# Kernel optimization log

Measured on AMD Instinct MI355X. Metric: run time of the kernel, lower is better.

Reference implementation:

```python
import jax, jax.numpy as jnp
import numpy as np

B, S, D = 4, 2048, 1024
H, DK, DV = 16, 64, 64
LN_EPS = 1e-5


def setup_inputs() -> dict:
    key = jax.random.key(0)
    ks = jax.random.split(key, 16)
    s = 0.02
    inp = {
        "Q": jax.random.normal(ks[0], (B, S, D), jnp.float32),
        "K": jax.random.normal(ks[1], (B, S, D), jnp.float32),
        "V": jax.random.normal(ks[2], (B, S, D), jnp.float32),
        "mask": jnp.tril(jnp.ones((S, S), jnp.int32)),  # causal 2D mask
        "W_Q": jax.random.normal(ks[3], (D, H * DK), jnp.float32) * s,
        "b_Q": jnp.zeros((H * DK,), jnp.float32),
        "W_K": jax.random.normal(ks[4], (D, H * DK), jnp.float32) * s,
        "b_K": jnp.zeros((H * DK,), jnp.float32),
        "W_V": jax.random.normal(ks[5], (D, H * DV), jnp.float32) * s,
        "b_V": jnp.zeros((H * DV,), jnp.float32),
        "W_O": jax.random.normal(ks[6], (H * DV, D), jnp.float32) * s,
        "b_O": jnp.zeros((D,), jnp.float32),
        "ln_gamma": jnp.ones((D,), jnp.float32),
        "ln_beta": jnp.zeros((D,), jnp.float32),
    }
    return inp


def reference(Q, K, V, mask, W_Q, b_Q, W_K, b_K, W_V, b_V, W_O, b_O, ln_gamma, ln_beta):
    residual = Q
    # projections -> [B, H, S, d]
    q = (Q @ W_Q + b_Q).reshape(B, S, H, DK).transpose(0, 2, 1, 3)
    k = (K @ W_K + b_K).reshape(B, S, H, DK).transpose(0, 2, 1, 3)
    v = (V @ W_V + b_V).reshape(B, S, H, DV).transpose(0, 2, 1, 3)
    # scaled dot-product attention with explicit [B,H,S,S] scores
    scores = jnp.einsum("bhqd,bhkd->bhqk", q, k) / jnp.sqrt(jnp.float32(DK))
    m = mask[None, None, :, :]  # 2D mask -> [1,1,S,S] as in torch code
    scores = jnp.where(m == 0, jnp.float32(-1e9), scores)
    attn = jax.nn.softmax(scores, axis=-1)
    out = jnp.einsum("bhqk,bhkd->bhqd", attn, v)
    out = out.transpose(0, 2, 1, 3).reshape(B, S, H * DV)
    out = out @ W_O + b_O
    # layer norm over residual + out
    x = residual + out
    mu = jnp.mean(x, axis=-1, keepdims=True)
    var = jnp.mean(jnp.square(x - mu), axis=-1, keepdims=True)
    y = (x - mu) / jnp.sqrt(var + LN_EPS) * ln_gamma + ln_beta
    return y, attn
```

## Files before the change

### kernel.cpp

```cpp
#include <hip/hip_runtime.h>
#include <hip/hip_bf16.h>
#include <math.h>

#define NB 4
#define NS 2048
#define ND 1024
#define NH 16

typedef __attribute__((ext_vector_type(8))) __bf16 bf16x8;
typedef __attribute__((ext_vector_type(4))) float f32x4;
typedef __attribute__((ext_vector_type(8))) unsigned short ushort8_t;

#define VMCNT0() asm volatile("s_waitcnt vmcnt(0)" ::: "memory")
#define VMCNT2() asm volatile("s_waitcnt vmcnt(2)" ::: "memory")
#define VMCNT4() asm volatile("s_waitcnt vmcnt(4)" ::: "memory")
#define LGKM0()  asm volatile("s_waitcnt lgkmcnt(0)" ::: "memory")
#define BAR()    __builtin_amdgcn_s_barrier()

__device__ __forceinline__ unsigned short f2bf(float f){
  union { float f; unsigned int u; } v; v.f = f;
  unsigned int r = (v.u + 0x7FFFu + ((v.u >> 16) & 1u)) >> 16;
  return (unsigned short)r;
}
__device__ __forceinline__ float bf2f(unsigned short u){
  union { unsigned int i; float f; } v; v.i = ((unsigned int)u) << 16;
  return v.f;
}
__device__ __forceinline__ f32x4 mfma16(bf16x8 a, bf16x8 b, f32x4 c){
  return __builtin_amdgcn_mfma_f32_16x16x32_bf16(a, b, c, 0, 0, 0);
}
__device__ __forceinline__ bf16x8 lds_frag(const unsigned short* p){
  ushort8_t u = *reinterpret_cast<const ushort8_t*>(p);
  return __builtin_bit_cast(bf16x8, u);
}
__device__ __forceinline__ void gl16(const unsigned short* g, unsigned short* l){
  __builtin_amdgcn_global_load_lds(
      (const __attribute__((address_space(1))) void*)g,
      (__attribute__((address_space(3))) void*)l, 16, 0, 0);
}

__global__ __launch_bounds__(256)
void k_convert3(const float* __restrict__ a, const float* __restrict__ b,
                const float* __restrict__ c, unsigned short* __restrict__ oa,
                unsigned short* __restrict__ ob, unsigned short* __restrict__ oc,
                int n4){
  int i = blockIdx.x * 256 + threadIdx.x;
  if (i >= n4) return;
  const float* in = (blockIdx.y == 0) ? a : (blockIdx.y == 1) ? b : c;
  unsigned short* out = (blockIdx.y == 0) ? oa : (blockIdx.y == 1) ? ob : oc;
  float4 v = reinterpret_cast<const float4*>(in)[i];
  ushort4 o;
  o.x = f2bf(v.x); o.y = f2bf(v.y); o.z = f2bf(v.z); o.w = f2bf(v.w);
  reinterpret_cast<ushort4*>(out)[i] = o;
}

__global__ __launch_bounds__(256)
void k_transpose4(const float* __restrict__ w0, const float* __restrict__ w1,
                  const float* __restrict__ w2, const float* __restrict__ w3,
                  unsigned short* __restrict__ out){
  __shared__ float t[32][33];
  const float* in = (blockIdx.z == 0) ? w0 : (blockIdx.z == 1) ? w1 :
                    (blockIdx.z == 2) ? w2 : w3;
  unsigned short* o = out + (size_t)blockIdx.z * 1048576;
  const int k0 = blockIdx.x * 32, n0 = blockIdx.y * 32;
  const int tx = threadIdx.x & 31, ty = threadIdx.x >> 5;
  for (int r = ty; r < 32; r += 8)
    t[r][tx] = in[(size_t)(k0 + r) * 1024 + n0 + tx];
  __syncthreads();
  for (int r = ty; r < 32; r += 8)
    o[(size_t)(n0 + r) * 1024 + k0 + tx] = f2bf(t[tx][r]);
}

__global__ __launch_bounds__(256)
void k_gemm_qkv(const unsigned short* __restrict__ A0,
                const unsigned short* __restrict__ A1,
                const unsigned short* __restrict__ A2,
                const unsigned short* __restrict__ WT,
                const float* __restrict__ b0, const float* __restrict__ b1,
                const float* __restrict__ b2,
                unsigned short* __restrict__ o0,
                unsigned short* __restrict__ o1,
                unsigned short* __restrict__ o2)
{
  constexpr int K = 1024;
  __shared__ unsigned short a_s[128 * 64];
  __shared__ unsigned short b_s[128 * 64];
  const int bm = blockIdx.x;
  const int gid = blockIdx.y >> 3, bn = blockIdx.y & 7;
  const unsigned short* A = (gid == 0) ? A0 : (gid == 1) ? A1 : A2;
  const unsigned short* BT = WT + (size_t)gid * 1048576;
  const float* bias = (gid == 0) ? b0 : (gid == 1) ? b1 : b2;
  unsigned short* outp = (gid == 0) ? o0 : (gid == 1) ? o1 : o2;

  const int tid = threadIdx.x, lane = tid & 63, w = tid >> 6;
  const int wr = w >> 1, wc = w & 1;
  const int l15 = lane & 15, l4 = lane >> 4;
  const int xsw = (l15 & 7) << 3;
  const int lr = lane >> 3;
  const int scol = ((lane & 7) << 3) ^ (lr << 3);

  const f32x4 z4 = {0.f, 0.f, 0.f, 0.f};
  f32x4 acc[4][4];
  #pragma unroll
  for (int i = 0; i < 4; ++i)
    #pragma unroll
    for (int j = 0; j < 4; ++j) acc[i][j] = z4;

  const size_t abase = (size_t)(bm * 128) * K;
  const size_t bbase = (size_t)(bn * 128) * K;

  for (int kt = 0; kt < 16; ++kt){
    __syncthreads();
    #pragma unroll
    for (int i = 0; i < 4; ++i){
      const int row = w * 32 + i * 8 + lr;
      gl16(&A[abase + (size_t)row * K + kt * 64 + scol], &a_s[(w * 32 + i * 8) * 64]);
      gl16(&BT[bbase + (size_t)row * K + kt * 64 + scol], &b_s[(w * 32 + i * 8) * 64]);
    }
    __syncthreads();
    #pragma unroll
    for (int ks = 0; ks < 2; ++ks){
      const int cb = (ks * 32 + l4 * 8) ^ xsw;
      bf16x8 af[4], bfr[4];
      #pragma unroll
      for (int mf = 0; mf < 4; ++mf)
        af[mf] = lds_frag(&a_s[(wr * 64 + mf * 16 + l15) * 64 + cb]);
      #pragma unroll
      for (int nf = 0; nf < 4; ++nf)
        bfr[nf] = lds_frag(&b_s[(wc * 64 + nf * 16 + l15) * 64 + cb]);
      #pragma unroll
      for (int mf = 0; mf < 4; ++mf)
        #pragma unroll
        for (int nf = 0; nf < 4; ++nf)
          acc[mf][nf] = mfma16(af[mf], bfr[nf], acc[mf][nf]);
    }
  }

  #pragma unroll
  for (int mf = 0; mf < 4; ++mf){
    #pragma unroll
    for (int nf = 0; nf < 4; ++nf){
      const int n = bn * 128 + wc * 64 + nf * 16 + l15;
      const float bv = bias[n];
      #pragma unroll
      for (int r = 0; r < 4; ++r){
        const int m = bm * 128 + wr * 64 + mf * 16 + l4 * 4 + r;
        const float v = acc[mf][nf][r] + bv;
        const int b = m >> 11, s = m & 2047, h = n >> 6, d = n & 63;
        if (gid <= 1)
          outp[((((size_t)b * NH + h) * NS + s) << 6) + d] = f2bf(v);
        else
          outp[(((size_t)b * NH + h) * 64 + d) * NS + s] = f2bf(v);
      }
    }
  }
}

__global__ __launch_bounds__(256)
void k_gemm_o(const unsigned short* __restrict__ A,
              const unsigned short* __restrict__ BT,
              const float* __restrict__ bias,
              const float* __restrict__ resid,
              unsigned short* __restrict__ outp)
{
  constexpr int K = 1024;
  __shared__ unsigned short a_s[128 * 64];
  __shared__ unsigned short b_s[128 * 64];
  const int bm = blockIdx.x, bn = blockIdx.y;
  const int tid = threadIdx.x, lane = tid & 63, w = tid >> 6;
  const int wr = w >> 1, wc = w & 1;
  const int l15 = lane & 15, l4 = lane >> 4;
  const int xsw = (l15 & 7) << 3;
  const int lr = lane >> 3;
  const int scol = ((lane & 7) << 3) ^ (lr << 3);

  const f32x4 z4 = {0.f, 0.f, 0.f, 0.f};
  f32x4 acc[4][4];
  #pragma unroll
  for (int i = 0; i < 4; ++i)
    #pragma unroll
    for (int j = 0; j < 4; ++j) acc[i][j] = z4;

  const size_t abase = (size_t)(bm * 128) * K;
  const size_t bbase = (size_t)(bn * 128) * K;

  for (int kt = 0; kt < 16; ++kt){
    __syncthreads();
    #pragma unroll
    for (int i = 0; i < 4; ++i){
      const int row = w * 32 + i * 8 + lr;
      gl16(&A[abase + (size_t)row * K + kt * 64 + scol], &a_s[(w * 32 + i * 8) * 64]);
      gl16(&BT[bbase + (size_t)row * K + kt * 64 + scol], &b_s[(w * 32 + i * 8) * 64]);
    }
    __syncthreads();
    #pragma unroll
    for (int ks = 0; ks < 2; ++ks){
      const int cb = (ks * 32 + l4 * 8) ^ xsw;
      bf16x8 af[4], bfr[4];
      #pragma unroll
      for (int mf = 0; mf < 4; ++mf)
        af[mf] = lds_frag(&a_s[(wr * 64 + mf * 16 + l15) * 64 + cb]);
      #pragma unroll
      for (int nf = 0; nf < 4; ++nf)
        bfr[nf] = lds_frag(&b_s[(wc * 64 + nf * 16 + l15) * 64 + cb]);
      #pragma unroll
      for (int mf = 0; mf < 4; ++mf)
        #pragma unroll
        for (int nf = 0; nf < 4; ++nf)
          acc[mf][nf] = mfma16(af[mf], bfr[nf], acc[mf][nf]);
    }
  }

  #pragma unroll
  for (int mf = 0; mf < 4; ++mf){
    #pragma unroll
    for (int nf = 0; nf < 4; ++nf){
      const int n = bn * 128 + wc * 64 + nf * 16 + l15;
      const float bv = bias[n];
      #pragma unroll
      for (int r = 0; r < 4; ++r){
        const int m = bm * 128 + wr * 64 + mf * 16 + l4 * 4 + r;
        const size_t idx = (size_t)m * ND + n;
        outp[idx] = f2bf(acc[mf][nf][r] + bv + resid[idx]);
      }
    }
  }
}

__global__ __launch_bounds__(256, 4)
void k_attn(const unsigned short* __restrict__ qh,
            const unsigned short* __restrict__ kh,
            const unsigned short* __restrict__ vt,
            unsigned short* __restrict__ ctx,
            float* __restrict__ attn)
{
  __shared__ unsigned short k_s0[64 * 64];
  __shared__ unsigned short k_s1[64 * 64];
  __shared__ unsigned short kv2[64 * 64];
  __shared__ unsigned short p_s[64][72];

  const int id = blockIdx.x + 32 * blockIdx.y;
  const int swz = (id & 7) * 256 + (id >> 3);
  const int bh = swz >> 5;
  const int qb = 31 - (swz & 31);
  const int q0 = qb * 64;
  const int tid = threadIdx.x, lane = tid & 63, w = tid >> 6;
  const int l15 = lane & 15, l4 = lane >> 4;
  const int xsw = (l15 & 7) << 3;
  const int lr = lane >> 3;
  const int scol = ((lane & 7) << 3) ^ (lr << 3);
  const f32x4 z4 = {0.f, 0.f, 0.f, 0.f};
  const size_t kvb = (size_t)bh * NS * 64;

  bf16x8 qf[2];
  {
    const unsigned short* qp = &qh[kvb + (size_t)(q0 + w * 16 + l15) * 64];
    qf[0] = lds_frag(qp + l4 * 8);
    qf[1] = lds_frag(qp + 32 + l4 * 8);
  }

  const float SC = 0.125f * 1.44269504088896341f;
  const int ncomp = qb + 1;
  const int growb = q0 + w * 16 + l4 * 4;

  float lp[4] = {0.f, 0.f, 0.f, 0.f};

  #pragma unroll
  for (int i = 0; i < 2; ++i)
    gl16(&kh[kvb + (size_t)(w * 16 + i * 8 + lr) * 64 + scol],
         &k_s0[(w * 16 + i * 8) * 64]);
  if (ncomp > 1){
    #pragma unroll
    for (int i = 0; i < 2; ++i)
      gl16(&kh[kvb + (size_t)(64 + w * 16 + i * 8 + lr) * 64 + scol],
           &k_s1[(w * 16 + i * 8) * 64]);
    VMCNT2();
  } else {
    VMCNT0();
  }
  BAR();

  int cbi = 0;
  for (int kt = 0; kt < ncomp; ++kt){
    const bool haveNext = (kt + 1 < ncomp);
    const bool havePre  = (kt + 2 < ncomp);
    if (havePre){
      int nbi = cbi + 2; if (nbi >= 3) nbi -= 3;
      unsigned short* nb = (nbi == 0) ? k_s0 : ((nbi == 1) ? k_s1 : kv2);
      #pragma unroll
      for (int i = 0; i < 2; ++i)
        gl16(&kh[kvb + (size_t)((kt + 2) * 64 + w * 16 + i * 8 + lr) * 64 + scol],
             &nb[(w * 16 + i * 8) * 64]);
    }
    const unsigned short* cb_ = (cbi == 0) ? k_s0 : ((cbi == 1) ? k_s1 : kv2);
    f32x4 sc4[4];
    #pragma unroll
    for (int cf = 0; cf < 4; ++cf) sc4[cf] = z4;
    __builtin_amdgcn_s_setprio(1);
    #pragma unroll
    for (int ks = 0; ks < 2; ++ks){
      const int cb = (ks * 32 + l4 * 8) ^ xsw;
      #pragma unroll
      for (int cf = 0; cf < 4; ++cf){
        const bf16x8 bk = lds_frag(&cb_[(cf * 16 + l15) * 64 + cb]);
        sc4[cf] = mfma16(qf[ks], bk, sc4[cf]);
      }
    }
    __builtin_amdgcn_s_setprio(0);
    if (kt == ncomp - 1){
      #pragma unroll
      for (int cf = 0; cf < 4; ++cf){
        const int gcol = kt * 64 + cf * 16 + l15;
        #pragma unroll
        for (int r = 0; r < 4; ++r)
          lp[r] += (gcol <= growb + r) ? exp2f(sc4[cf][r] * SC) : 0.f;
      }
    } else {
      #pragma unroll
      for (int cf = 0; cf < 4; ++cf)
        #pragma unroll
        for (int r = 0; r < 4; ++r)
          lp[r] += exp2f(sc4[cf][r] * SC);
    }
    if (havePre){ VMCNT2(); } else if (haveNext){ VMCNT0(); }
    LGKM0();
    BAR();
    cbi = (cbi == 2) ? 0 : cbi + 1;
  }

  float rl[4];
  #pragma unroll
  for (int r = 0; r < 4; ++r){
    float t = lp[r];
    t += __shfl_xor(t, 1);
    t += __shfl_xor(t, 2);
    t += __shfl_xor(t, 4);
    t += __shfl_xor(t, 8);
    rl[r] = 1.f / t;
  }

  f32x4 oacc[4];
  #pragma unroll
  for (int nf = 0; nf < 4; ++nf) oacc[nf] = z4;
  float* arow = attn + (size_t)bh * NS * NS;

  #pragma unroll
  for (int i = 0; i < 2; ++i)
    gl16(&kh[kvb + (size_t)(w * 16 + i * 8 + lr) * 64 + scol],
         &k_s0[(w * 16 + i * 8) * 64]);
  VMCNT0();
  BAR();
  int cur = 0;

  for (int kt = 0; kt < ncomp; ++kt){
    const bool haveK = (kt + 1 < ncomp);
    unsigned short* kcur = cur ? k_s1 : k_s0;
    unsigned short* knxt = cur ? k_s0 : k_s1;
    #pragma unroll
    for (int i = 0; i < 2; ++i){
      const int row = w * 16 + i * 8 + lr;
      gl16(&vt[kvb + (size_t)row * NS + kt * 64 + scol], &kv2[(w * 16 + i * 8) * 64]);
    }
    if (haveK){
      #pragma unroll
      for (int i = 0; i < 2; ++i)
        gl16(&kh[kvb + (size_t)((kt + 1) * 64 + w * 16 + i * 8 + lr) * 64 + scol],
             &knxt[(w * 16 + i * 8) * 64]);
    }
    f32x4 sc4[4];
    #pragma unroll
    for (int cf = 0; cf < 4; ++cf) sc4[cf] = z4;
    __builtin_amdgcn_s_setprio(1);
    #pragma unroll
    for (int ks = 0; ks < 2; ++ks){
      const int cb = (ks * 32 + l4 * 8) ^ xsw;
      #pragma unroll
      for (int cf = 0; cf < 4; ++cf){
        const bf16x8 bk = lds_frag(&kcur[(cf * 16 + l15) * 64 + cb]);
        sc4[cf] = mfma16(qf[ks], bk, sc4[cf]);
      }
    }
    __builtin_amdgcn_s_setprio(0);
    if (kt == ncomp - 1){
      #pragma unroll
      for (int cf = 0; cf < 4; ++cf){
        const int gcol = kt * 64 + cf * 16 + l15;
        #pragma unroll
        for (int r = 0; r < 4; ++r){
          const float a = (gcol <= growb + r) ? exp2f(sc4[cf][r] * SC) * rl[r] : 0.f;
          p_s[w * 16 + l4 * 4 + r][cf * 16 + l15] = f2bf(a);
        }
      }
    } else {
      #pragma unroll
      for (int cf = 0; cf < 4; ++cf)
        #pragma unroll
        for (int r = 0; r < 4; ++r)
          p_s[w * 16 + l4 * 4 + r][cf * 16 + l15] = f2bf(exp2f(sc4[cf][r] * SC) * rl[r]);
    }
    if (haveK){ VMCNT2(); } else { VMCNT0(); }
    LGKM0();
    BAR();
    #pragma unroll
    for (int it = 0; it < 4; ++it){
      const int row = it * 16 + (tid >> 4);
      const int c0 = (tid & 15) * 4;
      const ushort4 u = *reinterpret_cast<const ushort4*>(&p_s[row][c0]);
      float4 f4;
      f4.x = bf2f(u.x); f4.y = bf2f(u.y); f4.z = bf2f(u.z); f4.w = bf2f(u.w);
      *reinterpret_cast<float4*>(&arow[(size_t)(q0 + row) * NS + kt * 64 + c0]) = f4;
    }
    __builtin_amdgcn_s_setprio(1);
    #pragma unroll
    for (int ks2 = 0; ks2 < 2; ++ks2){
      const bf16x8 ap = lds_frag(&p_s[w * 16 + l15][ks2 * 32 + l4 * 8]);
      const int cb = (ks2 * 32 + l4 * 8) ^ xsw;
      #pragma unroll
      for (int nf = 0; nf < 4; ++nf){
        const bf16x8 bv = lds_frag(&kv2[(nf * 16 + l15) * 64 + cb]);
        oacc[nf] = mfma16(ap, bv, oacc[nf]);
      }
    }
    __builtin_amdgcn_s_setprio(0);
    if (haveK){
      VMCNT4();
      BAR();
    }
    cur ^= 1;
  }

  const int b = bh >> 4, h = bh & 15;
  #pragma unroll
  for (int nf = 0; nf < 4; ++nf){
    #pragma unroll
    for (int r = 0; r < 4; ++r){
      const int s = growb + r;
      ctx[((size_t)b * NS + s) * ND + h * 64 + nf * 16 + l15] = f2bf(oacc[nf][r]);
    }
  }

  const int zc0 = ncomp * 64;
  if (zc0 < NS){
    const float4 zz = make_float4(0.f, 0.f, 0.f, 0.f);
    for (int r = 0; r < 64; ++r){
      float* rp = arow + (size_t)(q0 + r) * NS;
      for (int c = zc0 + tid * 4; c < NS; c += 1024)
        *reinterpret_cast<float4*>(rp + c) = zz;
    }
  }
}

__global__ __launch_bounds__(256)
void k_ln(const unsigned short* __restrict__ x, const float* __restrict__ gamma,
          const float* __restrict__ beta, float* __restrict__ y){
  const int row = blockIdx.x;
  const ushort4 u = reinterpret_cast<const ushort4*>(x + (size_t)row * ND)[threadIdx.x];
  float v0 = bf2f(u.x), v1 = bf2f(u.y), v2 = bf2f(u.z), v3 = bf2f(u.w);
  float s = v0 + v1 + v2 + v3;
  float ss = v0 * v0 + v1 * v1 + v2 * v2 + v3 * v3;
  #pragma unroll
  for (int off = 32; off; off >>= 1){
    s += __shfl_xor(s, off);
    ss += __shfl_xor(ss, off);
  }
  __shared__ float rs[4], rss[4];
  const int w = threadIdx.x >> 6;
  if ((threadIdx.x & 63) == 0){ rs[w] = s; rss[w] = ss; }
  __syncthreads();
  s = rs[0] + rs[1] + rs[2] + rs[3];
  ss = rss[0] + rss[1] + rss[2] + rss[3];
  const float mu = s * (1.f / ND);
  const float var = ss * (1.f / ND) - mu * mu;
  const float rstd = rsqrtf(var + 1e-5f);
  const float4 g = reinterpret_cast<const float4*>(gamma)[threadIdx.x];
  const float4 be = reinterpret_cast<const float4*>(beta)[threadIdx.x];
  float4 o;
  o.x = (v0 - mu) * rstd * g.x + be.x;
  o.y = (v1 - mu) * rstd * g.y + be.y;
  o.z = (v2 - mu) * rstd * g.z + be.z;
  o.w = (v3 - mu) * rstd * g.w + be.w;
  reinterpret_cast<float4*>(y + (size_t)row * ND)[threadIdx.x] = o;
}

extern "C" void kernel_launch(void* const* d_in, const int* in_sizes, int n_in,
                              void* d_out, int out_size, void* d_ws, size_t ws_size,
                              hipStream_t stream){
  const float* Q   = (const float*)d_in[0];
  const float* Kin = (const float*)d_in[1];
  const float* V   = (const float*)d_in[2];
  const float* W_Q = (const float*)d_in[4];
  const float* b_Q = (const float*)d_in[5];
  const float* W_K = (const float*)d_in[6];
  const float* b_K = (const float*)d_in[7];
  const float* W_V = (const float*)d_in[8];
  const float* b_V = (const float*)d_in[9];
  const float* W_O = (const float*)d_in[10];
  const float* b_O = (const float*)d_in[11];
  const float* g   = (const float*)d_in[12];
  const float* be  = (const float*)d_in[13];

  char* ws = (char*)d_ws;
  const size_t SZ = (size_t)8192 * 1024 * 2;
  unsigned short* Qb = (unsigned short*)(ws);
  unsigned short* Kb = (unsigned short*)(ws + SZ);
  unsigned short* Vb = (unsigned short*)(ws + 2 * SZ);
  unsigned short* WT = (unsigned short*)(ws + 3 * SZ);
  unsigned short* qh = (unsigned short*)(ws + 3 * SZ + 4 * 2097152);
  unsigned short* kh = qh + (size_t)8388608;
  unsigned short* vt = kh + (size_t)8388608;
  unsigned short* ctx = Qb;
  unsigned short* x = Kb;
  float* y = (float*)d_out;
  float* attn = y + (size_t)NB * NS * ND;

  const int n4 = (NB * NS * ND) / 4;
  k_convert3<<<dim3(n4 / 256, 3), 256, 0, stream>>>(Q, Kin, V, Qb, Kb, Vb, n4);
  k_transpose4<<<dim3(32, 32, 4), 256, 0, stream>>>(W_Q, W_K, W_V, W_O, WT);

  k_gemm_qkv<<<dim3(64, 24), 256, 0, stream>>>(Qb, Kb, Vb, WT, b_Q, b_K, b_V,
                                               qh, kh, vt);

  k_attn<<<dim3(32, 64), 256, 0, stream>>>(qh, kh, vt, ctx, attn);

  k_gemm_o<<<dim3(64, 8), 256, 0, stream>>>(ctx, WT + 3 * 1048576, b_O, Q, x);

  k_ln<<<NB * NS, 256, 0, stream>>>(x, g, be, y);
}
```

Measured before the change: 428.3 us.

## Split attention into a row-statistics kernel and an output kernel

The fused attention kernel is split in two. The first kernel computes only the softmax row sums, using less LDS and a higher occupancy bound, and writes the reciprocals to a workspace buffer (reusing the Vb region). The second kernel loads those reciprocals, then writes the normalized attention probabilities and computes the context. This is meant to let the stats pass run at higher occupancy, at the cost of an extra launch, a global round-trip for the row statistics, and the Q/K fragment setup being repeated.

```diff
diff --git a/kernel.cpp b/kernel.cpp
--- a/kernel.cpp
+++ b/kernel.cpp
@@ -227,17 +227,14 @@
   }
 }
 
-__global__ __launch_bounds__(256, 4)
-void k_attn(const unsigned short* __restrict__ qh,
-            const unsigned short* __restrict__ kh,
-            const unsigned short* __restrict__ vt,
-            unsigned short* __restrict__ ctx,
-            float* __restrict__ attn)
+__global__ __launch_bounds__(256, 5)
+void k_attn_stats(const unsigned short* __restrict__ qh,
+                  const unsigned short* __restrict__ kh,
+                  float* __restrict__ rlbuf)
 {
   __shared__ unsigned short k_s0[64 * 64];
   __shared__ unsigned short k_s1[64 * 64];
-  __shared__ unsigned short kv2[64 * 64];
-  __shared__ unsigned short p_s[64][72];
+  __shared__ unsigned short k_s2[64 * 64];
 
   const int id = blockIdx.x + 32 * blockIdx.y;
   const int swz = (id & 7) * 256 + (id >> 3);
@@ -286,13 +283,13 @@
     const bool havePre  = (kt + 2 < ncomp);
     if (havePre){
       int nbi = cbi + 2; if (nbi >= 3) nbi -= 3;
-      unsigned short* nb = (nbi == 0) ? k_s0 : ((nbi == 1) ? k_s1 : kv2);
+      unsigned short* nb = (nbi == 0) ? k_s0 : ((nbi == 1) ? k_s1 : k_s2);
       #pragma unroll
       for (int i = 0; i < 2; ++i)
         gl16(&kh[kvb + (size_t)((kt + 2) * 64 + w * 16 + i * 8 + lr) * 64 + scol],
              &nb[(w * 16 + i * 8) * 64]);
     }
-    const unsigned short* cb_ = (cbi == 0) ? k_s0 : ((cbi == 1) ? k_s1 : kv2);
+    const unsigned short* cb_ = (cbi == 0) ? k_s0 : ((cbi == 1) ? k_s1 : k_s2);
     f32x4 sc4[4];
     #pragma unroll
     for (int cf = 0; cf < 4; ++cf) sc4[cf] = z4;
@@ -328,7 +325,6 @@
     cbi = (cbi == 2) ? 0 : cbi + 1;
   }
 
-  float rl[4];
   #pragma unroll
   for (int r = 0; r < 4; ++r){
     float t = lp[r];
@@ -336,8 +332,52 @@
     t += __shfl_xor(t, 2);
     t += __shfl_xor(t, 4);
     t += __shfl_xor(t, 8);
-    rl[r] = 1.f / t;
-  }
+    if (l15 == 0)
+      rlbuf[(size_t)bh * NS + growb + r] = 1.f / t;
+  }
+}
+
+__global__ __launch_bounds__(256, 4)
+void k_attn_out(const unsigned short* __restrict__ qh,
+                const unsigned short* __restrict__ kh,
+                const unsigned short* __restrict__ vt,
+                const float* __restrict__ rlbuf,
+                unsigned short* __restrict__ ctx,
+                float* __restrict__ attn)
+{
+  __shared__ unsigned short k_s0[64 * 64];
+  __shared__ unsigned short k_s1[64 * 64];
+  __shared__ unsigned short kv2[64 * 64];
+  __shared__ unsigned short p_s[64][72];
+
+  const int id = blockIdx.x + 32 * blockIdx.y;
+  const int swz = (id & 7) * 256 + (id >> 3);
+  const int bh = swz >> 5;
+  const int qb = 31 - (swz & 31);
+  const int q0 = qb * 64;
+  const int tid = threadIdx.x, lane = tid & 63, w = tid >> 6;
+  const int l15 = lane & 15, l4 = lane >> 4;
+  const int xsw = (l15 & 7) << 3;
+  const int lr = lane >> 3;
+  const int scol = ((lane & 7) << 3) ^ (lr << 3);
+  const f32x4 z4 = {0.f, 0.f, 0.f, 0.f};
+  const size_t kvb = (size_t)bh * NS * 64;
+
+  bf16x8 qf[2];
+  {
+    const unsigned short* qp = &qh[kvb + (size_t)(q0 + w * 16 + l15) * 64];
+    qf[0] = lds_frag(qp + l4 * 8);
+    qf[1] = lds_frag(qp + 32 + l4 * 8);
+  }
+
+  const float SC = 0.125f * 1.44269504088896341f;
+  const int ncomp = qb + 1;
+  const int growb = q0 + w * 16 + l4 * 4;
+
+  float rl[4];
+  #pragma unroll
+  for (int r = 0; r < 4; ++r)
+    rl[r] = rlbuf[(size_t)bh * NS + growb + r];
 
   f32x4 oacc[4];
   #pragma unroll
@@ -510,6 +550,7 @@
   unsigned short* vt = kh + (size_t)8388608;
   unsigned short* ctx = Qb;
   unsigned short* x = Kb;
+  float* rlbuf = (float*)(ws + 2 * SZ);
   float* y = (float*)d_out;
   float* attn = y + (size_t)NB * NS * ND;
 
@@ -520,7 +561,8 @@
   k_gemm_qkv<<<dim3(64, 24), 256, 0, stream>>>(Qb, Kb, Vb, WT, b_Q, b_K, b_V,
                                                qh, kh, vt);
 
-  k_attn<<<dim3(32, 64), 256, 0, stream>>>(qh, kh, vt, ctx, attn);
+  k_attn_stats<<<dim3(32, 64), 256, 0, stream>>>(qh, kh, rlbuf);
+  k_attn_out<<<dim3(32, 64), 256, 0, stream>>>(qh, kh, vt, rlbuf, ctx, attn);
 
   k_gemm_o<<<dim3(64, 8), 256, 0, stream>>>(ctx, WT + 3 * 1048576, b_O, Q, x);
 
```

Result: slower. 479.2 us (+11.9%).
